# Kernel tuning notes

Hardware: AMD Instinct MI355X
Metric: run time of the kernel (lower is better)

Reference implementation:

```python
import jax, jax.numpy as jnp
import numpy as np

B, T, C, NH = 8, 1024, 768, 12

def setup_inputs() -> dict:
    key = jax.random.key(0)
    k1, k2, k3 = jax.random.split(key, 3)
    x = jax.random.normal(k1, (B, T, C), dtype=jnp.float32)
    Wqkv = jax.random.normal(k2, (C, 3 * C), dtype=jnp.float32) * 0.02
    bqkv = jnp.zeros((3 * C,), dtype=jnp.float32)
    Wproj = jax.random.normal(k3, (C, C), dtype=jnp.float32) * 0.02
    bproj = jnp.zeros((C,), dtype=jnp.float32)
    return {"x": x, "Wqkv": Wqkv, "bqkv": bqkv, "Wproj": Wproj, "bproj": bproj}

def reference(x, Wqkv, bqkv, Wproj, bproj):
    b, t, c = x.shape
    hs = c // NH
    qkv = x @ Wqkv + bqkv  # [B,T,3C]
    q, k, v = jnp.split(qkv, 3, axis=2)
    # [B,T,C] -> [B,NH,T,hs]
    q = q.reshape(b, t, NH, hs).transpose(0, 2, 1, 3)
    k = k.reshape(b, t, NH, hs).transpose(0, 2, 1, 3)
    v = v.reshape(b, t, NH, hs).transpose(0, 2, 1, 3)
    att = jnp.einsum('bhqd,bhkd->bhqk', q, k) * (hs ** -0.5)
    causal = jnp.tril(jnp.ones((t, t), dtype=bool))
    att = jnp.where(causal[None, None], att, jnp.finfo(att.dtype).min)
    att = jax.nn.softmax(att, axis=-1)
    y = jnp.einsum('bhqk,bhkd->bhqd', att, v)
    y = y.transpose(0, 2, 1, 3).reshape(b, t, c)
    return y @ Wproj + bproj
```

## Files before the change

### kernel.cpp

```cpp
#include <hip/hip_runtime.h>

constexpr int Bb  = 8;
constexpr int Tt  = 1024;
constexpr int Cc  = 768;
constexpr int NHh = 12;
constexpr int HS  = 64;
constexpr int C3  = 3 * Cc;

typedef short bf16x8 __attribute__((ext_vector_type(8)));
typedef float f32x4  __attribute__((ext_vector_type(4)));

__device__ inline short bf16r(float f) {
    unsigned u = __float_as_uint(f);
    u += 0x7FFF + ((u >> 16) & 1);
    return (short)(u >> 16);
}
__device__ inline short bf16h(float f) {
    return (short)((__float_as_uint(f) + 0x8000u) >> 16);
}

__global__ __launch_bounds__(256)
void f32_to_bf16(const float* __restrict__ in, short* __restrict__ out, int n) {
    int i = (blockIdx.x * 256 + threadIdx.x) * 4;
    if (i < n) {
        float4 v = *(const float4*)(in + i);
        short4 o;
        o.x = bf16r(v.x); o.y = bf16r(v.y); o.z = bf16r(v.z); o.w = bf16r(v.w);
        *(short4*)(out + i) = o;
    }
}

__global__ __launch_bounds__(1024)
void transpose_to_bf16(const float* __restrict__ in, short* __restrict__ out,
                       int R, int C) {
    __shared__ short tile[32][33];
    int c = blockIdx.x * 32 + threadIdx.x;
    int r = blockIdx.y * 32 + threadIdx.y;
    tile[threadIdx.y][threadIdx.x] = bf16r(in[(size_t)r * C + c]);
    __syncthreads();
    int oc   = blockIdx.y * 32 + threadIdx.x;
    int orow = blockIdx.x * 32 + threadIdx.y;
    out[(size_t)orow * R + oc] = tile[threadIdx.x][threadIdx.y];
}

__global__ __launch_bounds__(256)
void transpose_v(const short* __restrict__ qkv, short* __restrict__ vt) {
    __shared__ short tile[64][65];
    const int bh = blockIdx.y;
    const int b = bh / NHh, h = bh % NHh;
    const int t0 = blockIdx.x * 64;
    const int tx = threadIdx.x & 63, ty = threadIdx.x >> 6;
    const short* src = qkv + ((size_t)b * Tt + t0) * C3 + 2 * Cc + h * HS;
#pragma unroll
    for (int r = 0; r < 16; ++r)
        tile[ty * 16 + r][tx] = src[(size_t)(ty * 16 + r) * C3 + tx];
    __syncthreads();
    short* dst = vt + (size_t)bh * HS * Tt + t0;
#pragma unroll
    for (int r = 0; r < 16; ++r)
        dst[(size_t)(ty * 16 + r) * Tt + tx] = tile[tx][ty * 16 + r];
}

template <int OB>
__global__ __launch_bounds__(256)
void gemm_mfma_bias(const short* __restrict__ A, const short* __restrict__ Bt,
                    const float* __restrict__ bias, void* __restrict__ Cout,
                    int M, int N, int K) {
    __shared__ short Als[128 * 32];
    __shared__ short Bls[128 * 32];

    const int t = threadIdx.x, w = t >> 6, lane = t & 63;
    const int m0 = blockIdx.y * 128, n0 = blockIdx.x * 128;

    const int r0 = (t * 16) >> 6;
    const int c0 = ((t * 16) & 63) >> 1;
    const short* Ag0 = A  + (size_t)(m0 + r0)      * K + c0;
    const short* Ag1 = A  + (size_t)(m0 + r0 + 64) * K + c0;
    const short* Bg0 = Bt + (size_t)(n0 + r0)      * K + c0;
    const short* Bg1 = Bt + (size_t)(n0 + r0 + 64) * K + c0;
    char* AlsBase = (char*)Als + w * 1024;
    char* BlsBase = (char*)Bls + w * 1024;

    const int wm = (w >> 1) * 64, wn = (w & 1) * 64;
    const int laneM = lane & 15, laneK = (lane >> 4) * 8;

    f32x4 acc[4][4] = {};

    for (int kt = 0; kt < K; kt += 32) {
        __syncthreads();
        __builtin_amdgcn_global_load_lds(
            (const __attribute__((address_space(1))) void*)(Ag0 + kt),
            (__attribute__((address_space(3))) void*)(AlsBase), 16, 0, 0);
        __builtin_amdgcn_global_load_lds(
            (const __attribute__((address_space(1))) void*)(Ag1 + kt),
            (__attribute__((address_space(3))) void*)(AlsBase + 4096), 16, 0, 0);
        __builtin_amdgcn_global_load_lds(
            (const __attribute__((address_space(1))) void*)(Bg0 + kt),
            (__attribute__((address_space(3))) void*)(BlsBase), 16, 0, 0);
        __builtin_amdgcn_global_load_lds(
            (const __attribute__((address_space(1))) void*)(Bg1 + kt),
            (__attribute__((address_space(3))) void*)(BlsBase + 4096), 16, 0, 0);
        __syncthreads();

        bf16x8 af[4], bfr[4];
#pragma unroll
        for (int i = 0; i < 4; ++i) {
            af[i]  = *(const bf16x8*)&Als[(wm + i * 16 + laneM) * 32 + laneK];
            bfr[i] = *(const bf16x8*)&Bls[(wn + i * 16 + laneM) * 32 + laneK];
        }
#pragma unroll
        for (int i = 0; i < 4; ++i)
#pragma unroll
            for (int j = 0; j < 4; ++j)
                acc[i][j] = __builtin_amdgcn_mfma_f32_16x16x32_bf16(
                    af[i], bfr[j], acc[i][j], 0, 0, 0);
    }

    const int rowBase = m0 + wm + (lane >> 4) * 4;
    const int colBase = n0 + wn + laneM;
#pragma unroll
    for (int j = 0; j < 4; ++j) {
        const int col = colBase + j * 16;
        const float bv = bias[col];
#pragma unroll
        for (int i = 0; i < 4; ++i) {
#pragma unroll
            for (int r = 0; r < 4; ++r) {
                const int row = rowBase + i * 16 + r;
                const float v = acc[i][j][r] + bv;
                if (OB) ((short*)Cout)[(size_t)row * N + col] = bf16r(v);
                else    ((float*)Cout)[(size_t)row * N + col] = v;
            }
        }
    }
}

__global__ __launch_bounds__(256)
void flash_attn(const short* __restrict__ qkv, const short* __restrict__ vt,
                short* __restrict__ y) {
    const int bh = blockIdx.x % (Bb * NHh);
    const int pi = blockIdx.x / (Bb * NHh);
    const int h  = bh % NHh, b = bh / NHh;
    const int t = threadIdx.x, w = t >> 6, lane = t & 63;
    const int laneM = lane & 15, laneG = lane >> 4;

    __shared__ short Kls[64 * 64];
    __shared__ short Vls[64 * 64];
    __shared__ short Pls[4][16 * 72];

    const size_t bT = (size_t)b * Tt;

    bf16x8 onesb;
#pragma unroll
    for (int j = 0; j < 8; ++j) onesb[j] = (short)0x3F80;

    const int srow = t >> 3;
    const int gpos = t & 7;
    char* KlsB = (char*)Kls + w * 1024;
    char* VlsB = (char*)Vls + w * 1024;
    const int gs0 = (gpos ^ (srow & 7)) * 8;

    const short* Kbase = qkv + (bT + srow) * C3 + Cc + h * HS + gs0;
    const short* Vbase = vt + ((size_t)bh * HS + srow) * Tt + gs0;

    constexpr float cexp = 0.18033688f;
    constexpr float moff = -5.7707801f;

#pragma unroll 1
    for (int sub = 0; sub < 2; ++sub) {
        const int qt = sub ? (15 - pi) : pi;
        const int q0 = qt * 64;

        const short* qp = qkv + (bT + q0 + w * 16 + laneM) * C3 + h * HS;
        const bf16x8 qf0 = *(const bf16x8*)(qp + laneG * 8);
        const bf16x8 qf1 = *(const bf16x8*)(qp + 32 + laneG * 8);

        f32x4 oacc[4] = {};
        f32x4 lacc   = {};

        const short* Kg = Kbase;
        const short* Vg = Vbase;
#pragma unroll 1
        for (int kt = 0; kt <= qt; ++kt, Kg += 64 * C3, Vg += 64) {
            __syncthreads();
            __builtin_amdgcn_global_load_lds(
                (const __attribute__((address_space(1))) void*)Kg,
                (__attribute__((address_space(3))) void*)(KlsB), 16, 0, 0);
            __builtin_amdgcn_global_load_lds(
                (const __attribute__((address_space(1))) void*)(Kg + 32 * C3),
                (__attribute__((address_space(3))) void*)(KlsB + 4096), 16, 0, 0);
            __builtin_amdgcn_global_load_lds(
                (const __attribute__((address_space(1))) void*)Vg,
                (__attribute__((address_space(3))) void*)(VlsB), 16, 0, 0);
            __builtin_amdgcn_global_load_lds(
                (const __attribute__((address_space(1))) void*)(Vg + 32 * Tt),
                (__attribute__((address_space(3))) void*)(VlsB + 4096), 16, 0, 0);
            __syncthreads();

            f32x4 sacc[4] = {};
#pragma unroll
            for (int ks = 0; ks < 2; ++ks) {
                const bf16x8 qf = ks ? qf1 : qf0;
#pragma unroll
                for (int nb = 0; nb < 4; ++nb) {
                    const int key = nb * 16 + laneM;
                    const bf16x8 kf = *(const bf16x8*)
                        &Kls[key * 64 + (((ks << 2) + laneG) ^ (key & 7)) * 8];
                    sacc[nb] = __builtin_amdgcn_mfma_f32_16x16x32_bf16(
                        qf, kf, sacc[nb], 0, 0, 0);
                }
            }

            if (kt == qt) {
#pragma unroll
                for (int nb = 0; nb < 4; ++nb) {
                    const int col = nb * 16 + laneM;
#pragma unroll
                    for (int r = 0; r < 4; ++r) {
                        const int row = w * 16 + laneG * 4 + r;
                        if (col > row) sacc[nb][r] = -1e30f;
                    }
                }
            }

            short* Pw = &Pls[w][0];
#pragma unroll
            for (int r = 0; r < 4; ++r)
#pragma unroll
                for (int nb = 0; nb < 4; ++nb) {
                    const float pv = exp2f(fmaf(sacc[nb][r], cexp, moff));
                    Pw[(laneG * 4 + r) * 72 + nb * 16 + laneM] = bf16h(pv);
                }

#pragma unroll
            for (int ks = 0; ks < 2; ++ks) {
                const bf16x8 pf = *(const bf16x8*)&Pw[laneM * 72 + ks * 32 + laneG * 8];
                lacc = __builtin_amdgcn_mfma_f32_16x16x32_bf16(pf, onesb, lacc, 0, 0, 0);
#pragma unroll
                for (int nb = 0; nb < 4; ++nb) {
                    const int d = nb * 16 + laneM;
                    const bf16x8 vf = *(const bf16x8*)
                        &Vls[d * 64 + (((ks << 2) + laneG) ^ (d & 7)) * 8];
                    oacc[nb] = __builtin_amdgcn_mfma_f32_16x16x32_bf16(
                        pf, vf, oacc[nb], 0, 0, 0);
                }
            }
        }

        short* yp = y + (bT + q0 + w * 16) * Cc + h * HS;
#pragma unroll
        for (int r = 0; r < 4; ++r) {
            const float inv = 1.f / lacc[r];
#pragma unroll
            for (int nb = 0; nb < 4; ++nb)
                yp[(size_t)(laneG * 4 + r) * Cc + nb * 16 + laneM] = bf16r(oacc[nb][r] * inv);
        }
    }
}

extern "C" void kernel_launch(void* const* d_in, const int* in_sizes, int n_in,
                              void* d_out, int out_size, void* d_ws, size_t ws_size,
                              hipStream_t stream) {
    const float* x     = (const float*)d_in[0];
    const float* Wqkv  = (const float*)d_in[1];
    const float* bqkv  = (const float*)d_in[2];
    const float* Wproj = (const float*)d_in[3];
    const float* bproj = (const float*)d_in[4];

    constexpr int M = Bb * Tt;
    short* xb     = (short*)d_ws;
    short* wqkvT  = xb     + (size_t)M * Cc;
    short* wprojT = wqkvT  + (size_t)C3 * Cc;
    short* qkv    = wprojT + (size_t)Cc * Cc;
    short* yatt   = qkv    + (size_t)M * C3;
    short* vt     = yatt   + (size_t)M * Cc;

    f32_to_bf16<<<dim3((M * Cc) / 1024), dim3(256), 0, stream>>>(x, xb, M * Cc);
    transpose_to_bf16<<<dim3(C3 / 32, Cc / 32), dim3(32, 32), 0, stream>>>(Wqkv, wqkvT, Cc, C3);
    transpose_to_bf16<<<dim3(Cc / 32, Cc / 32), dim3(32, 32), 0, stream>>>(Wproj, wprojT, Cc, Cc);

    gemm_mfma_bias<1><<<dim3(C3 / 128, M / 128), dim3(256), 0, stream>>>(
        xb, wqkvT, bqkv, qkv, M, C3, Cc);

    transpose_v<<<dim3(Tt / 64, Bb * NHh), dim3(256), 0, stream>>>(qkv, vt);

    flash_attn<<<dim3(Bb * NHh * 8), dim3(256), 0, stream>>>(qkv, vt, yatt);

    gemm_mfma_bias<0><<<dim3(Cc / 128, M / 128), dim3(256), 0, stream>>>(
        yatt, wprojT, bproj, (float*)d_out, M, Cc, Cc);
}
```

Before: 204.2 us.

## Deepen GEMM K-tile to 64 with XOR-swizzled LDS and smaller proj M-tile

The bias GEMM now stages a 64-wide K slice per iteration, which halves the barrier and load-issue rounds. The LDS layout uses an XOR swizzle on 16-byte groups to avoid bank conflicts on the fragment reads. The kernel is templated on the M tile size: the QKV GEMM keeps 128 rows and the output projection uses 64 rows, doubling its block count for better CU occupancy. LDS use per block doubles, and fewer tiles per wave in the projection lowers operand reuse.

After: 199.2 us. -2.5%, faster.

```diff
diff --git a/kernel.cpp b/kernel.cpp
--- a/kernel.cpp
+++ b/kernel.cpp
@@ -61,69 +61,79 @@
         dst[(size_t)(ty * 16 + r) * Tt + tx] = tile[tx][ty * 16 + r];
 }
 
-template <int OB>
+template <int MI, int OB>
 __global__ __launch_bounds__(256)
 void gemm_mfma_bias(const short* __restrict__ A, const short* __restrict__ Bt,
                     const float* __restrict__ bias, void* __restrict__ Cout,
                     int M, int N, int K) {
-    __shared__ short Als[128 * 32];
-    __shared__ short Bls[128 * 32];
+    constexpr int TM = MI * 32;
+    __shared__ short Als[TM * 64];
+    __shared__ short Bls[128 * 64];
 
     const int t = threadIdx.x, w = t >> 6, lane = t & 63;
-    const int m0 = blockIdx.y * 128, n0 = blockIdx.x * 128;
-
-    const int r0 = (t * 16) >> 6;
-    const int c0 = ((t * 16) & 63) >> 1;
-    const short* Ag0 = A  + (size_t)(m0 + r0)      * K + c0;
-    const short* Ag1 = A  + (size_t)(m0 + r0 + 64) * K + c0;
-    const short* Bg0 = Bt + (size_t)(n0 + r0)      * K + c0;
-    const short* Bg1 = Bt + (size_t)(n0 + r0 + 64) * K + c0;
-    char* AlsBase = (char*)Als + w * 1024;
-    char* BlsBase = (char*)Bls + w * 1024;
-
-    const int wm = (w >> 1) * 64, wn = (w & 1) * 64;
-    const int laneM = lane & 15, laneK = (lane >> 4) * 8;
-
-    f32x4 acc[4][4] = {};
-
-    for (int kt = 0; kt < K; kt += 32) {
+    const int m0 = blockIdx.y * TM, n0 = blockIdx.x * 128;
+
+    const int sr = t >> 3;
+    const int sg = ((t & 7) ^ (sr & 7)) * 8;
+
+    const short* Ag[MI];
+#pragma unroll
+    for (int q = 0; q < MI; ++q)
+        Ag[q] = A + (size_t)(m0 + q * 32 + sr) * K + sg;
+    const short* Bg[4];
+#pragma unroll
+    for (int q = 0; q < 4; ++q)
+        Bg[q] = Bt + (size_t)(n0 + q * 32 + sr) * K + sg;
+
+    char* AlsB = (char*)Als + w * 1024;
+    char* BlsB = (char*)Bls + w * 1024;
+
+    const int wm = (w >> 1) * (MI * 16), wn = (w & 1) * 64;
+    const int laneM = lane & 15, laneG = lane >> 4;
+
+    f32x4 acc[MI][4] = {};
+
+    for (int kt = 0; kt < K; kt += 64) {
         __syncthreads();
-        __builtin_amdgcn_global_load_lds(
-            (const __attribute__((address_space(1))) void*)(Ag0 + kt),
-            (__attribute__((address_space(3))) void*)(AlsBase), 16, 0, 0);
-        __builtin_amdgcn_global_load_lds(
-            (const __attribute__((address_space(1))) void*)(Ag1 + kt),
-            (__attribute__((address_space(3))) void*)(AlsBase + 4096), 16, 0, 0);
-        __builtin_amdgcn_global_load_lds(
-            (const __attribute__((address_space(1))) void*)(Bg0 + kt),
-            (__attribute__((address_space(3))) void*)(BlsBase), 16, 0, 0);
-        __builtin_amdgcn_global_load_lds(
-            (const __attribute__((address_space(1))) void*)(Bg1 + kt),
-            (__attribute__((address_space(3))) void*)(BlsBase + 4096), 16, 0, 0);
+#pragma unroll
+        for (int q = 0; q < MI; ++q)
+            __builtin_amdgcn_global_load_lds(
+                (const __attribute__((address_space(1))) void*)(Ag[q] + kt),
+                (__attribute__((address_space(3))) void*)(AlsB + q * 4096), 16, 0, 0);
+#pragma unroll
+        for (int q = 0; q < 4; ++q)
+            __builtin_amdgcn_global_load_lds(
+                (const __attribute__((address_space(1))) void*)(Bg[q] + kt),
+                (__attribute__((address_space(3))) void*)(BlsB + q * 4096), 16, 0, 0);
         __syncthreads();
 
-        bf16x8 af[4], bfr[4];
-#pragma unroll
-        for (int i = 0; i < 4; ++i) {
-            af[i]  = *(const bf16x8*)&Als[(wm + i * 16 + laneM) * 32 + laneK];
-            bfr[i] = *(const bf16x8*)&Bls[(wn + i * 16 + laneM) * 32 + laneK];
+#pragma unroll
+        for (int ks = 0; ks < 2; ++ks) {
+            const int kx = (((ks << 2) + laneG) ^ (laneM & 7)) * 8;
+            bf16x8 af[MI], bfr[4];
+#pragma unroll
+            for (int i = 0; i < MI; ++i)
+                af[i] = *(const bf16x8*)&Als[(wm + i * 16 + laneM) * 64 + kx];
+#pragma unroll
+            for (int j = 0; j < 4; ++j)
+                bfr[j] = *(const bf16x8*)&Bls[(wn + j * 16 + laneM) * 64 + kx];
+#pragma unroll
+            for (int i = 0; i < MI; ++i)
+#pragma unroll
+                for (int j = 0; j < 4; ++j)
+                    acc[i][j] = __builtin_amdgcn_mfma_f32_16x16x32_bf16(
+                        af[i], bfr[j], acc[i][j], 0, 0, 0);
         }
-#pragma unroll
-        for (int i = 0; i < 4; ++i)
-#pragma unroll
-            for (int j = 0; j < 4; ++j)
-                acc[i][j] = __builtin_amdgcn_mfma_f32_16x16x32_bf16(
-                    af[i], bfr[j], acc[i][j], 0, 0, 0);
     }
 
-    const int rowBase = m0 + wm + (lane >> 4) * 4;
+    const int rowBase = m0 + wm + laneG * 4;
     const int colBase = n0 + wn + laneM;
 #pragma unroll
     for (int j = 0; j < 4; ++j) {
         const int col = colBase + j * 16;
         const float bv = bias[col];
 #pragma unroll
-        for (int i = 0; i < 4; ++i) {
+        for (int i = 0; i < MI; ++i) {
 #pragma unroll
             for (int r = 0; r < 4; ++r) {
                 const int row = rowBase + i * 16 + r;
@@ -279,13 +289,13 @@
     transpose_to_bf16<<<dim3(C3 / 32, Cc / 32), dim3(32, 32), 0, stream>>>(Wqkv, wqkvT, Cc, C3);
     transpose_to_bf16<<<dim3(Cc / 32, Cc / 32), dim3(32, 32), 0, stream>>>(Wproj, wprojT, Cc, Cc);
 
-    gemm_mfma_bias<1><<<dim3(C3 / 128, M / 128), dim3(256), 0, stream>>>(
+    gemm_mfma_bias<4, 1><<<dim3(C3 / 128, M / 128), dim3(256), 0, stream>>>(
         xb, wqkvT, bqkv, qkv, M, C3, Cc);
 
     transpose_v<<<dim3(Tt / 64, Bb * NHh), dim3(256), 0, stream>>>(qkv, vt);
 
     flash_attn<<<dim3(Bb * NHh * 8), dim3(256), 0, stream>>>(qkv, vt, yatt);
 
-    gemm_mfma_bias<0><<<dim3(Cc / 128, M / 128), dim3(256), 0, stream>>>(
+    gemm_mfma_bias<2, 0><<<dim3(Cc / 128, M / 64), dim3(256), 0, stream>>>(
         yatt, wprojT, bproj, (float*)d_out, M, Cc, Cc);
 }
```
